# Optimization experiments

Hardware: AMD Instinct MI355X
Metric: run time of the kernel (lower is better)

The kernel has to match this reference:

```python
import jax, jax.numpy as jnp
import numpy as np

B, D = 8192, 1024          # batch, input dim
UNITS = [1024, 512]        # expert MLP hidden sizes
T, E_T, E_S = 2, 2, 4      # num_tasks, experts per task, shared experts
E = T * E_T + E_S          # total experts = 8


def setup_inputs() -> dict:
    key = jax.random.key(0)
    k = jax.random.split(key, 6)
    H, O = UNITS
    x = jax.random.normal(k[0], (B, D), dtype=jnp.float32)
    # glorot-normal-ish scaling for expert weights
    W1 = jax.random.normal(k[1], (E, D, H), dtype=jnp.float32) * np.sqrt(2.0 / (D + H))
    b1 = jnp.zeros((E, H), dtype=jnp.float32)
    W2 = jax.random.normal(k[2], (E, H, O), dtype=jnp.float32) * np.sqrt(2.0 / (H + O))
    b2 = jnp.zeros((E, O), dtype=jnp.float32)
    # per-task gate over (E_T + E_S) experts, no bias (use_bias=False in Dense)
    Wg = jax.random.normal(k[3], (T, D, E_T + E_S), dtype=jnp.float32) * np.sqrt(2.0 / (D + E_T + E_S))
    # shared gate over all E experts
    Wgs = jax.random.normal(k[4], (D, E), dtype=jnp.float32) * np.sqrt(2.0 / (D + E))
    return {"x": x, "W1": W1, "b1": b1, "W2": W2, "b2": b2, "Wg": Wg, "Wgs": Wgs}


def reference(x, W1, b1, W2, b2, Wg, Wgs):
    # All experts see the same input (2D-input path of CGC3: tf.tile over experts).
    # Batched grouped GEMM over the expert axis instead of a Python loop.
    h = jax.nn.relu(jnp.einsum('bd,edh->ebh', x, W1) + b1[:, None, :])   # [E,B,H]
    eo = jax.nn.relu(jnp.einsum('ebh,eho->ebo', h, W2) + b2[:, None, :]) # [E,B,O]

    outs = []
    for i in range(T):
        # experts for task i = its own E_T experts + the last E_S shared experts
        idx = jnp.array(list(range(i * E_T, (i + 1) * E_T)) + list(range(E - E_S, E)))
        g = jax.nn.softmax(x @ Wg[i], axis=-1)            # [B, E_T+E_S]
        sel = eo[idx]                                     # [E_T+E_S, B, O]
        outs.append(jnp.einsum('be,ebo->bo', g, sel))     # [B, O]
    # output_share=True: share tower gated over all experts
    gs = jax.nn.softmax(x @ Wgs, axis=-1)                 # [B, E]
    outs.append(jnp.einsum('be,ebo->bo', gs, eo))         # [B, O]
    return jnp.stack(outs, axis=1)                        # [B, T+1, O]
```

## Files before the change

### kernel.cpp

```cpp
#include <hip/hip_runtime.h>
#include <hip/hip_bf16.h>
#include <stdint.h>

#define B_SZ 8192
#define D_SZ 1024
#define H_SZ 1024
#define O_SZ 512
#define E_SZ 8

typedef float f32x4 __attribute__((ext_vector_type(4)));
typedef __bf16 bf16x8 __attribute__((ext_vector_type(8)));

typedef __attribute__((address_space(1))) uint32_t gu32;
typedef __attribute__((address_space(3))) uint32_t lu32;

__device__ __forceinline__ unsigned short f2bf(float f) {
    union { __hip_bfloat16 h; unsigned short u; } c;
    c.h = __float2bfloat16(f);
    return c.u;
}
__device__ __forceinline__ float bf2f(unsigned short u) {
    union { float f; uint32_t u; } c;
    c.u = ((uint32_t)u) << 16;
    return c.f;
}

__global__ __launch_bounds__(256) void k_convert_gates(const float* __restrict__ x,
                                                       const float* __restrict__ Wg,
                                                       const float* __restrict__ Wgs,
                                                       unsigned short* __restrict__ x_bf,
                                                       float* __restrict__ g_all) {
    const int wv = threadIdx.x >> 6;
    const int lane = threadIdx.x & 63;
    const int b = blockIdx.x * 4 + wv;
    const float* xr = x + (size_t)b * D_SZ;
    unsigned short* xo = x_bf + (size_t)b * D_SZ;
    float acc[20];
#pragma unroll
    for (int j = 0; j < 20; ++j) acc[j] = 0.f;
#pragma unroll 4
    for (int it = 0; it < 16; ++it) {
        const int d = it * 64 + lane;
        const float xv = xr[d];
        xo[d] = f2bf(xv);
        const float* w0 = Wg + (size_t)d * 6;
        const float* w1 = Wg + (size_t)D_SZ * 6 + (size_t)d * 6;
        const float* ws = Wgs + (size_t)d * 8;
#pragma unroll
        for (int j = 0; j < 6; ++j) acc[j] += xv * w0[j];
#pragma unroll
        for (int j = 0; j < 6; ++j) acc[6 + j] += xv * w1[j];
#pragma unroll
        for (int j = 0; j < 8; ++j) acc[12 + j] += xv * ws[j];
    }
#pragma unroll
    for (int j = 0; j < 20; ++j) {
        float v = acc[j];
#pragma unroll
        for (int s = 32; s > 0; s >>= 1) v += __shfl_down(v, s, 64);
        acc[j] = v;
    }
    if (lane == 0) {
        float* g = g_all + (size_t)b * 20;
#pragma unroll
        for (int t = 0; t < 3; ++t) {
            int base = (t == 0) ? 0 : (t == 1 ? 6 : 12);
            int cnt  = (t == 2) ? 8 : 6;
            float m = -1e30f;
            for (int j = 0; j < cnt; ++j) m = fmaxf(m, acc[base + j]);
            float ex[8]; float sum = 0.f;
            for (int j = 0; j < cnt; ++j) { ex[j] = __expf(acc[base + j] - m); sum += ex[j]; }
            float inv = 1.f / sum;
            for (int j = 0; j < cnt; ++j) g[base + j] = ex[j] * inv;
        }
    }
}

__global__ __launch_bounds__(512) void k_transpose_convert(const float* __restrict__ in,
                                                           unsigned short* __restrict__ out,
                                                           int R, int C) {
    __shared__ float tile[64][65];
    const float* src = in + (size_t)blockIdx.z * R * C;
    unsigned short* dst = out + (size_t)blockIdx.z * R * C;
    int c0 = blockIdx.x * 64, r0 = blockIdx.y * 64;
    int tx = threadIdx.x, ty = threadIdx.y;
#pragma unroll
    for (int rr = ty; rr < 64; rr += 8)
        tile[rr][tx] = src[(size_t)(r0 + rr) * C + c0 + tx];
    __syncthreads();
#pragma unroll
    for (int rr = ty; rr < 64; rr += 8)
        dst[(size_t)(c0 + rr) * R + r0 + tx] = f2bf(tile[tx][rr]);
}

__global__ __launch_bounds__(512, 2) void k_gemm_pipe(
    const unsigned short* __restrict__ A,
    const unsigned short* __restrict__ Bt,
    const float* __restrict__ bias,
    unsigned short* __restrict__ C,
    int M, int N, int K,
    long long sA, long long sB, long long sBias, long long sC, int e_base) {

    const int tid = threadIdx.x;
    const int lane = tid & 63, wid = tid >> 6;
    const int wr = wid >> 2, wc = wid & 3;
    const int lr = lane & 15, lg = lane >> 4;

    const int nwg = gridDim.x;
    const int wg = blockIdx.x;
    const int swz = (wg & 7) * (nwg >> 3) + (wg >> 3);
    const int nx = N >> 8;
    const int my = M >> 8;
    const int bx = swz % nx;
    const int t1 = swz / nx;
    const int by = t1 % my;
    const int e  = t1 / my + e_base;

    A    += (size_t)((long long)e * sA);
    Bt   += (size_t)((long long)e * sB);
    bias += (size_t)((long long)e * sBias);
    C    += (size_t)((long long)e * sC);

    const int m0 = by * 256, n0 = bx * 256;

    __shared__ __align__(16) unsigned short lds[65536];
    char* ldsb = (char*)lds;

    const int srow = tid >> 2;
    const int scol = (((tid & 3) ^ ((tid >> 3) & 3)) * 8);
    const int sdst = tid * 16;

    auto stageA2 = [&](int t) {
        const int bb = (t & 3) * 32768;
        const unsigned short* s0 = A + (size_t)(m0 + srow) * K + (t << 5) + scol;
        __builtin_amdgcn_global_load_lds((gu32*)s0, (lu32*)(ldsb + bb + sdst), 16, 0, 0);
        __builtin_amdgcn_global_load_lds((gu32*)(s0 + (size_t)128 * K),
                                         (lu32*)(ldsb + bb + 8192 + sdst), 16, 0, 0);
    };
    auto stageB2 = [&](int t) {
        const int bb = (t & 3) * 32768 + 16384;
        const unsigned short* s0 = Bt + (size_t)(n0 + srow) * K + (t << 5) + scol;
        __builtin_amdgcn_global_load_lds((gu32*)s0, (lu32*)(ldsb + bb + sdst), 16, 0, 0);
        __builtin_amdgcn_global_load_lds((gu32*)(s0 + (size_t)128 * K),
                                         (lu32*)(ldsb + bb + 8192 + sdst), 16, 0, 0);
    };

    const int cblk = (lg ^ ((lr >> 1) & 3)) * 16;
    const int aoff = wr * 8192 + lr * 64 + cblk;
    const int boff = 16384 + (wc >> 1) * 8192 + (wc & 1) * 4096 + lr * 64 + cblk;

    f32x4 acc[8][4];
#pragma unroll
    for (int i = 0; i < 8; ++i)
#pragma unroll
        for (int j = 0; j < 4; ++j)
            acc[i][j] = f32x4{0.f, 0.f, 0.f, 0.f};

    auto mfma16 = [&](const bf16x8 (&fa)[4], const bf16x8 (&fb)[4], int rbase) {
        __builtin_amdgcn_s_setprio(1);
#pragma unroll
        for (int i = 0; i < 4; ++i)
#pragma unroll
            for (int j = 0; j < 4; ++j)
                acc[rbase + i][j] = __builtin_amdgcn_mfma_f32_16x16x32_bf16(
                    fa[i], fb[j], acc[rbase + i][j], 0, 0, 0);
        __builtin_amdgcn_s_setprio(0);
    };

    const int NT = K >> 5;

    stageA2(0); stageB2(0); stageA2(1); stageB2(1); stageA2(2); stageB2(2);
    asm volatile("s_waitcnt vmcnt(8)" ::: "memory");
    asm volatile("s_barrier" ::: "memory");

    bf16x8 aU0[4], aL0[4], b0[4], aU1[4], aL1[4], b1v[4];
#pragma unroll
    for (int i = 0; i < 4; ++i) aU0[i] = *(const bf16x8*)(ldsb + aoff + i * 1024);
#pragma unroll
    for (int j = 0; j < 4; ++j) b0[j]  = *(const bf16x8*)(ldsb + boff + j * 1024);

    for (int t = 0; t < NT; t += 2) {
        const int bb0 = (t & 3) * 32768;
        const int bb1 = ((t + 1) & 3) * 32768;
        const int bb2 = ((t + 2) & 3) * 32768;

#pragma unroll
        for (int i = 0; i < 4; ++i) aL0[i] = *(const bf16x8*)(ldsb + bb0 + aoff + (4 + i) * 1024);
        if (t + 2 < NT) { asm volatile("s_waitcnt vmcnt(4)" ::: "memory"); }
        else            { asm volatile("s_waitcnt vmcnt(0)" ::: "memory"); }
        asm volatile("s_barrier" ::: "memory");
        if (t + 3 < NT) stageA2(t + 3);
        mfma16(aU0, b0, 0);

#pragma unroll
        for (int i = 0; i < 4; ++i) aU1[i] = *(const bf16x8*)(ldsb + bb1 + aoff + i * 1024);
#pragma unroll
        for (int j = 0; j < 4; ++j) b1v[j] = *(const bf16x8*)(ldsb + bb1 + boff + j * 1024);
        asm volatile("s_barrier" ::: "memory");
        if (t + 3 < NT) stageB2(t + 3);
        mfma16(aL0, b0, 4);

#pragma unroll
        for (int i = 0; i < 4; ++i) aL1[i] = *(const bf16x8*)(ldsb + bb1 + aoff + (4 + i) * 1024);
        if (t + 3 < NT) { asm volatile("s_waitcnt vmcnt(4)" ::: "memory"); }
        else            { asm volatile("s_waitcnt vmcnt(0)" ::: "memory"); }
        asm volatile("s_barrier" ::: "memory");
        if (t + 4 < NT) stageA2(t + 4);
        mfma16(aU1, b1v, 0);

        if (t + 2 < NT) {
#pragma unroll
            for (int i = 0; i < 4; ++i) aU0[i] = *(const bf16x8*)(ldsb + bb2 + aoff + i * 1024);
#pragma unroll
            for (int j = 0; j < 4; ++j) b0[j]  = *(const bf16x8*)(ldsb + bb2 + boff + j * 1024);
        }
        asm volatile("s_barrier" ::: "memory");
        if (t + 4 < NT) stageB2(t + 4);
        mfma16(aL1, b1v, 4);
    }

    __syncthreads();
    unsigned short* ct = (unsigned short*)ldsb;
#pragma unroll
    for (int j = 0; j < 4; ++j) {
        const int nn = wc * 64 + j * 16 + lr;
        const float bv = bias[n0 + nn];
#pragma unroll
        for (int i = 0; i < 8; ++i) {
            const int mb = wr * 128 + i * 16 + lg * 4;
#pragma unroll
            for (int r = 0; r < 4; ++r) {
                float v = fmaxf(acc[i][j][r] + bv, 0.f);
                ct[(size_t)(mb + r) * 256 + nn] = f2bf(v);
            }
        }
    }
    __syncthreads();
#pragma unroll
    for (int it = 0; it < 16; ++it) {
        const int row = it * 16 + (tid >> 5);
        const int colE = (tid & 31) * 8;
        *(int4*)(&C[(size_t)(m0 + row) * N + n0 + colE]) =
            *(const int4*)(ldsb + it * 8192 + (size_t)tid * 16);
    }
}

__global__ __launch_bounds__(256) void k_combine(const unsigned short* __restrict__ eo,
                                                 const float* __restrict__ g_all,
                                                 float* __restrict__ out) {
    int idx4 = blockIdx.x * 256 + threadIdx.x;
    int b = idx4 >> 7;
    int o4 = (idx4 & 127) * 4;
    const float* g = g_all + (size_t)b * 20;
    float v[E_SZ][4];
#pragma unroll
    for (int e = 0; e < E_SZ; ++e) {
        ushort4 u = *(const ushort4*)(eo + (size_t)e * B_SZ * O_SZ + (size_t)b * O_SZ + o4);
        v[e][0] = bf2f(u.x); v[e][1] = bf2f(u.y); v[e][2] = bf2f(u.z); v[e][3] = bf2f(u.w);
    }
    float4 r0, r1, r2;
    float* p0 = (float*)&r0; float* p1 = (float*)&r1; float* p2 = (float*)&r2;
#pragma unroll
    for (int c = 0; c < 4; ++c) {
        p0[c] = g[0] * v[0][c] + g[1] * v[1][c] + g[2] * v[4][c] + g[3] * v[5][c]
              + g[4] * v[6][c] + g[5] * v[7][c];
        p1[c] = g[6] * v[2][c] + g[7] * v[3][c] + g[8] * v[4][c] + g[9] * v[5][c]
              + g[10] * v[6][c] + g[11] * v[7][c];
        float s = 0.f;
#pragma unroll
        for (int e = 0; e < E_SZ; ++e) s += g[12 + e] * v[e][c];
        p2[c] = s;
    }
    size_t ob = (size_t)b * (3 * O_SZ) + o4;
    *(float4*)(out + ob) = r0;
    *(float4*)(out + ob + O_SZ) = r1;
    *(float4*)(out + ob + 2 * O_SZ) = r2;
}

extern "C" void kernel_launch(void* const* d_in, const int* in_sizes, int n_in,
                              void* d_out, int out_size, void* d_ws, size_t ws_size,
                              hipStream_t stream) {
    const float* x   = (const float*)d_in[0];
    const float* W1  = (const float*)d_in[1];
    const float* b1  = (const float*)d_in[2];
    const float* W2  = (const float*)d_in[3];
    const float* b2  = (const float*)d_in[4];
    const float* Wg  = (const float*)d_in[5];
    const float* Wgs = (const float*)d_in[6];
    float* out = (float*)d_out;

    char* ws = (char*)d_ws;
    const size_t SZ_XBF  = (size_t)B_SZ * D_SZ * 2;
    const size_t SZ_W1T  = (size_t)E_SZ * H_SZ * D_SZ * 2;
    const size_t SZ_W2T  = (size_t)E_SZ * O_SZ * H_SZ * 2;
    const size_t SZ_EO   = (size_t)E_SZ * B_SZ * O_SZ * 2;
    const size_t SZ_G    = (size_t)B_SZ * 20 * 4;
    const size_t SZ_HBIG = (size_t)E_SZ * B_SZ * H_SZ * 2;

    unsigned short* x_bf = (unsigned short*)ws;              ws += SZ_XBF;
    unsigned short* W1T  = (unsigned short*)ws;              ws += SZ_W1T;
    unsigned short* W2T  = (unsigned short*)ws;              ws += SZ_W2T;
    unsigned short* eo   = (unsigned short*)ws;              ws += SZ_EO;
    float* g_all         = (float*)ws;                       ws += SZ_G;
    unsigned short* h_buf = (unsigned short*)ws;

    const size_t fixed = SZ_XBF + SZ_W1T + SZ_W2T + SZ_EO + SZ_G;
    const bool big = ws_size >= fixed + SZ_HBIG;

    k_convert_gates<<<B_SZ / 4, 256, 0, stream>>>(x, Wg, Wgs, x_bf, g_all);
    dim3 tb(64, 8);
    k_transpose_convert<<<dim3(H_SZ / 64, D_SZ / 64, E_SZ), tb, 0, stream>>>(W1, W1T, D_SZ, H_SZ);
    k_transpose_convert<<<dim3(O_SZ / 64, H_SZ / 64, E_SZ), tb, 0, stream>>>(W2, W2T, H_SZ, O_SZ);

    if (big) {
        k_gemm_pipe<<<(H_SZ / 256) * (B_SZ / 256) * E_SZ, 512, 0, stream>>>(
            x_bf, W1T, b1, h_buf, B_SZ, H_SZ, D_SZ,
            0LL, (long long)H_SZ * D_SZ, (long long)H_SZ, (long long)B_SZ * H_SZ, 0);
        k_gemm_pipe<<<(O_SZ / 256) * (B_SZ / 256) * E_SZ, 512, 0, stream>>>(
            h_buf, W2T, b2, eo, B_SZ, O_SZ, H_SZ,
            (long long)B_SZ * H_SZ, (long long)O_SZ * H_SZ, (long long)O_SZ, (long long)B_SZ * O_SZ, 0);
    } else {
        for (int e = 0; e < E_SZ; ++e) {
            k_gemm_pipe<<<(H_SZ / 256) * (B_SZ / 256), 512, 0, stream>>>(
                x_bf, W1T, b1, h_buf, B_SZ, H_SZ, D_SZ,
                0LL, (long long)H_SZ * D_SZ, (long long)H_SZ, 0LL, e);
            k_gemm_pipe<<<(O_SZ / 256) * (B_SZ / 256), 512, 0, stream>>>(
                h_buf, W2T, b2, eo, B_SZ, O_SZ, H_SZ,
                0LL, (long long)O_SZ * H_SZ, (long long)O_SZ, (long long)B_SZ * O_SZ, e);
        }
    }

    k_combine<<<(B_SZ * O_SZ / 4) / 256, 256, 0, stream>>>(eo, g_all, out);
}
```

Baseline: 307.0 us.

## Use k-blocked panel layouts for GEMM operands and switch to 32x32x16 MFMA

Stores x, the transposed weights and the hidden activations in a panel layout (256-row panels of 8-element k-blocks), so each GEMM tile stage is one contiguous load into LDS. It also replaces the 16x16x32 MFMA tiles with 32x32x16 ones, using fewer, larger accumulators. The first GEMM now writes its output in panel layout through a swizzled LDS staging area so the second GEMM can read it the same way. The aim is cheaper global-to-LDS traffic and fewer LDS fragment reads per MFMA. The LDS read patterns change and may bring bank conflicts, and the layouts of all producers and consumers must agree exactly.

```diff
diff --git a/kernel.cpp b/kernel.cpp
--- a/kernel.cpp
+++ b/kernel.cpp
@@ -8,7 +8,7 @@
 #define O_SZ 512
 #define E_SZ 8
 
-typedef float f32x4 __attribute__((ext_vector_type(4)));
+typedef float f32x16 __attribute__((ext_vector_type(16)));
 typedef __bf16 bf16x8 __attribute__((ext_vector_type(8)));
 
 typedef __attribute__((address_space(1))) uint32_t gu32;
@@ -25,16 +25,18 @@
     return c.f;
 }
 
-__global__ __launch_bounds__(256) void k_convert_gates(const float* __restrict__ x,
-                                                       const float* __restrict__ Wg,
-                                                       const float* __restrict__ Wgs,
-                                                       unsigned short* __restrict__ x_bf,
-                                                       float* __restrict__ g_all) {
+
+__global__ __launch_bounds__(1024) void k_convert_gates(const float* __restrict__ x,
+                                                        const float* __restrict__ Wg,
+                                                        const float* __restrict__ Wgs,
+                                                        unsigned short* __restrict__ x_kb,
+                                                        float* __restrict__ g_all) {
+    __shared__ unsigned short xs[16][D_SZ];
     const int wv = threadIdx.x >> 6;
     const int lane = threadIdx.x & 63;
-    const int b = blockIdx.x * 4 + wv;
+    const int b0 = blockIdx.x * 16;
+    const int b = b0 + wv;
     const float* xr = x + (size_t)b * D_SZ;
-    unsigned short* xo = x_bf + (size_t)b * D_SZ;
     float acc[20];
 #pragma unroll
     for (int j = 0; j < 20; ++j) acc[j] = 0.f;
@@ -42,7 +44,7 @@
     for (int it = 0; it < 16; ++it) {
         const int d = it * 64 + lane;
         const float xv = xr[d];
-        xo[d] = f2bf(xv);
+        xs[wv][d] = f2bf(xv);
         const float* w0 = Wg + (size_t)d * 6;
         const float* w1 = Wg + (size_t)D_SZ * 6 + (size_t)d * 6;
         const float* ws = Wgs + (size_t)d * 8;
@@ -74,11 +76,21 @@
             for (int j = 0; j < cnt; ++j) g[base + j] = ex[j] * inv;
         }
     }
-}
-
-__global__ __launch_bounds__(512) void k_transpose_convert(const float* __restrict__ in,
-                                                           unsigned short* __restrict__ out,
-                                                           int R, int C) {
+    __syncthreads();
+    const char* lb = (const char*)&xs[0][0];
+#pragma unroll
+    for (int p = 0; p < 2; ++p) {
+        const int u = p * 1024 + threadIdx.x;
+        const int kblk = u >> 4, r16 = u & 15;
+        int4 v = *(const int4*)(lb + r16 * 2048 + kblk * 16);
+        *(int4*)(x_kb + (size_t)(b0 >> 8) * (D_SZ * 256) + (size_t)kblk * 2048
+                 + ((b0 & 255) + r16) * 8) = v;
+    }
+}
+
+__global__ __launch_bounds__(512) void k_transpose_panel(const float* __restrict__ in,
+                                                         unsigned short* __restrict__ out,
+                                                         int R, int C) {
     __shared__ float tile[64][65];
     const float* src = in + (size_t)blockIdx.z * R * C;
     unsigned short* dst = out + (size_t)blockIdx.z * R * C;
@@ -88,12 +100,17 @@
     for (int rr = ty; rr < 64; rr += 8)
         tile[rr][tx] = src[(size_t)(r0 + rr) * C + c0 + tx];
     __syncthreads();
-#pragma unroll
-    for (int rr = ty; rr < 64; rr += 8)
-        dst[(size_t)(c0 + rr) * R + r0 + tx] = f2bf(tile[tx][rr]);
-}
-
-__global__ __launch_bounds__(512, 2) void k_gemm_pipe(
+    union { ushort4 h[2]; int4 q; } u;
+#pragma unroll
+    for (int s = 0; s < 8; ++s)
+        ((unsigned short*)&u)[s] = f2bf(tile[ty * 8 + s][tx]);
+    const int c = c0 + tx;
+    *(int4*)(dst + (size_t)(c >> 8) * (R * 256) + (size_t)((r0 >> 3) + ty) * 2048
+             + (c & 255) * 8) = u.q;
+}
+
+template <bool PANEL_OUT>
+__global__ __launch_bounds__(512, 2) void k_gemm_p(
     const unsigned short* __restrict__ A,
     const unsigned short* __restrict__ Bt,
     const float* __restrict__ bias,
@@ -104,7 +121,7 @@
     const int tid = threadIdx.x;
     const int lane = tid & 63, wid = tid >> 6;
     const int wr = wid >> 2, wc = wid & 3;
-    const int lr = lane & 15, lg = lane >> 4;
+    const int lr32 = lane & 31, hi = lane >> 5;
 
     const int nwg = gridDim.x;
     const int wg = blockIdx.x;
@@ -126,122 +143,142 @@
     __shared__ __align__(16) unsigned short lds[65536];
     char* ldsb = (char*)lds;
 
-    const int srow = tid >> 2;
-    const int scol = (((tid & 3) ^ ((tid >> 3) & 3)) * 8);
-    const int sdst = tid * 16;
-
-    auto stageA2 = [&](int t) {
-        const int bb = (t & 3) * 32768;
-        const unsigned short* s0 = A + (size_t)(m0 + srow) * K + (t << 5) + scol;
-        __builtin_amdgcn_global_load_lds((gu32*)s0, (lu32*)(ldsb + bb + sdst), 16, 0, 0);
-        __builtin_amdgcn_global_load_lds((gu32*)(s0 + (size_t)128 * K),
-                                         (lu32*)(ldsb + bb + 8192 + sdst), 16, 0, 0);
-    };
-    auto stageB2 = [&](int t) {
-        const int bb = (t & 3) * 32768 + 16384;
-        const unsigned short* s0 = Bt + (size_t)(n0 + srow) * K + (t << 5) + scol;
-        __builtin_amdgcn_global_load_lds((gu32*)s0, (lu32*)(ldsb + bb + sdst), 16, 0, 0);
-        __builtin_amdgcn_global_load_lds((gu32*)(s0 + (size_t)128 * K),
-                                         (lu32*)(ldsb + bb + 8192 + sdst), 16, 0, 0);
-    };
-
-    const int cblk = (lg ^ ((lr >> 1) & 3)) * 16;
-    const int aoff = wr * 8192 + lr * 64 + cblk;
-    const int boff = 16384 + (wc >> 1) * 8192 + (wc & 1) * 4096 + lr * 64 + cblk;
-
-    f32x4 acc[8][4];
-#pragma unroll
-    for (int i = 0; i < 8; ++i)
-#pragma unroll
-        for (int j = 0; j < 4; ++j)
-            acc[i][j] = f32x4{0.f, 0.f, 0.f, 0.f};
-
-    auto mfma16 = [&](const bf16x8 (&fa)[4], const bf16x8 (&fb)[4], int rbase) {
+    const int skb = tid >> 8;
+    const int srw = tid & 255;
+
+    auto stageA = [&](int tt) {
+        const int bb = (tt & 3) * 32768;
+        const unsigned short* s0 = A + (size_t)(m0 >> 8) * K * 256
+                                     + (size_t)(tt * 4 + skb) * 2048 + srw * 8;
+        __builtin_amdgcn_global_load_lds((gu32*)s0, (lu32*)(ldsb + bb + tid * 16), 16, 0, 0);
+        __builtin_amdgcn_global_load_lds((gu32*)(s0 + 4096),
+                                         (lu32*)(ldsb + bb + 8192 + tid * 16), 16, 0, 0);
+    };
+    auto stageB = [&](int tt) {
+        const int bb = (tt & 3) * 32768 + 16384;
+        const unsigned short* s0 = Bt + (size_t)(n0 >> 8) * K * 256
+                                      + (size_t)(tt * 4 + skb) * 2048 + srw * 8;
+        __builtin_amdgcn_global_load_lds((gu32*)s0, (lu32*)(ldsb + bb + tid * 16), 16, 0, 0);
+        __builtin_amdgcn_global_load_lds((gu32*)(s0 + 4096),
+                                         (lu32*)(ldsb + bb + 8192 + tid * 16), 16, 0, 0);
+    };
+
+    const int abase = (wr * 128 + lr32) * 16 + hi * 4096;
+    const int bbase = 16384 + (wc * 64 + lr32) * 16 + hi * 4096;
+
+    auto readA = [&](bf16x8* d, int bb, int mb) {
+#pragma unroll
+        for (int q = 0; q < 4; ++q) {
+            const int mi = mb + (q >> 1), s = q & 1;
+            d[q] = *(const bf16x8*)(ldsb + bb + abase + mi * 512 + s * 8192);
+        }
+    };
+    auto readB = [&](bf16x8* d, int bb) {
+#pragma unroll
+        for (int q = 0; q < 4; ++q) {
+            const int nj = q >> 1, s = q & 1;
+            d[q] = *(const bf16x8*)(ldsb + bb + bbase + nj * 512 + s * 8192);
+        }
+    };
+
+    f32x16 acc[4][2];
+#pragma unroll
+    for (int i = 0; i < 4; ++i)
+#pragma unroll
+        for (int j = 0; j < 2; ++j)
+            acc[i][j] = (f32x16)(0.f);
+
+    auto mfma8 = [&](const bf16x8* fa, const bf16x8* fb, int rb) {
         __builtin_amdgcn_s_setprio(1);
 #pragma unroll
-        for (int i = 0; i < 4; ++i)
-#pragma unroll
-            for (int j = 0; j < 4; ++j)
-                acc[rbase + i][j] = __builtin_amdgcn_mfma_f32_16x16x32_bf16(
-                    fa[i], fb[j], acc[rbase + i][j], 0, 0, 0);
+        for (int i = 0; i < 2; ++i)
+#pragma unroll
+            for (int j = 0; j < 2; ++j)
+#pragma unroll
+                for (int s = 0; s < 2; ++s)
+                    acc[rb + i][j] = __builtin_amdgcn_mfma_f32_32x32x16_bf16(
+                        fa[i * 2 + s], fb[j * 2 + s], acc[rb + i][j], 0, 0, 0);
         __builtin_amdgcn_s_setprio(0);
     };
 
     const int NT = K >> 5;
 
-    stageA2(0); stageB2(0); stageA2(1); stageB2(1); stageA2(2); stageB2(2);
+    stageA(0); stageB(0); stageA(1); stageB(1); stageA(2); stageB(2);
     asm volatile("s_waitcnt vmcnt(8)" ::: "memory");
     asm volatile("s_barrier" ::: "memory");
 
     bf16x8 aU0[4], aL0[4], b0[4], aU1[4], aL1[4], b1v[4];
-#pragma unroll
-    for (int i = 0; i < 4; ++i) aU0[i] = *(const bf16x8*)(ldsb + aoff + i * 1024);
-#pragma unroll
-    for (int j = 0; j < 4; ++j) b0[j]  = *(const bf16x8*)(ldsb + boff + j * 1024);
+    readA(aU0, 0, 0); readB(b0, 0);
 
     for (int t = 0; t < NT; t += 2) {
         const int bb0 = (t & 3) * 32768;
         const int bb1 = ((t + 1) & 3) * 32768;
         const int bb2 = ((t + 2) & 3) * 32768;
 
-#pragma unroll
-        for (int i = 0; i < 4; ++i) aL0[i] = *(const bf16x8*)(ldsb + bb0 + aoff + (4 + i) * 1024);
+        readA(aL0, bb0, 2);
         if (t + 2 < NT) { asm volatile("s_waitcnt vmcnt(4)" ::: "memory"); }
         else            { asm volatile("s_waitcnt vmcnt(0)" ::: "memory"); }
         asm volatile("s_barrier" ::: "memory");
-        if (t + 3 < NT) stageA2(t + 3);
-        mfma16(aU0, b0, 0);
-
-#pragma unroll
-        for (int i = 0; i < 4; ++i) aU1[i] = *(const bf16x8*)(ldsb + bb1 + aoff + i * 1024);
-#pragma unroll
-        for (int j = 0; j < 4; ++j) b1v[j] = *(const bf16x8*)(ldsb + bb1 + boff + j * 1024);
+        if (t + 3 < NT) stageA(t + 3);
+        mfma8(aU0, b0, 0);
+
+        readA(aU1, bb1, 0); readB(b1v, bb1);
         asm volatile("s_barrier" ::: "memory");
-        if (t + 3 < NT) stageB2(t + 3);
-        mfma16(aL0, b0, 4);
-
-#pragma unroll
-        for (int i = 0; i < 4; ++i) aL1[i] = *(const bf16x8*)(ldsb + bb1 + aoff + (4 + i) * 1024);
+        if (t + 3 < NT) stageB(t + 3);
+        mfma8(aL0, b0, 2);
+
+        readA(aL1, bb1, 2);
         if (t + 3 < NT) { asm volatile("s_waitcnt vmcnt(4)" ::: "memory"); }
         else            { asm volatile("s_waitcnt vmcnt(0)" ::: "memory"); }
         asm volatile("s_barrier" ::: "memory");
-        if (t + 4 < NT) stageA2(t + 4);
-        mfma16(aU1, b1v, 0);
-
-        if (t + 2 < NT) {
-#pragma unroll
-            for (int i = 0; i < 4; ++i) aU0[i] = *(const bf16x8*)(ldsb + bb2 + aoff + i * 1024);
-#pragma unroll
-            for (int j = 0; j < 4; ++j) b0[j]  = *(const bf16x8*)(ldsb + bb2 + boff + j * 1024);
-        }
+        if (t + 4 < NT) stageA(t + 4);
+        mfma8(aU1, b1v, 0);
+
+        if (t + 2 < NT) { readA(aU0, bb2, 0); readB(b0, bb2); }
         asm volatile("s_barrier" ::: "memory");
-        if (t + 4 < NT) stageB2(t + 4);
-        mfma16(aL1, b1v, 4);
+        if (t + 4 < NT) stageB(t + 4);
+        mfma8(aL1, b1v, 4 - 2);
     }
 
     __syncthreads();
     unsigned short* ct = (unsigned short*)ldsb;
 #pragma unroll
-    for (int j = 0; j < 4; ++j) {
-        const int nn = wc * 64 + j * 16 + lr;
+    for (int nj = 0; nj < 2; ++nj) {
+        const int nn = wc * 64 + nj * 32 + lr32;
         const float bv = bias[n0 + nn];
 #pragma unroll
-        for (int i = 0; i < 8; ++i) {
-            const int mb = wr * 128 + i * 16 + lg * 4;
-#pragma unroll
-            for (int r = 0; r < 4; ++r) {
-                float v = fmaxf(acc[i][j][r] + bv, 0.f);
-                ct[(size_t)(mb + r) * 256 + nn] = f2bf(v);
+        for (int mi = 0; mi < 4; ++mi) {
+#pragma unroll
+            for (int r = 0; r < 16; ++r) {
+                const int mloc = wr * 128 + mi * 32 + (r & 3) + 8 * (r >> 2) + 4 * hi;
+                float v = fmaxf(acc[mi][nj][r] + bv, 0.f);
+                if (PANEL_OUT) {
+                    const int pu = (nn >> 3) ^ (mloc & 7);
+                    *(unsigned short*)(ldsb + mloc * 512 + pu * 16 + (nn & 7) * 2) = f2bf(v);
+                } else {
+                    ct[(size_t)mloc * 256 + nn] = f2bf(v);
+                }
             }
         }
     }
     __syncthreads();
-#pragma unroll
-    for (int it = 0; it < 16; ++it) {
-        const int row = it * 16 + (tid >> 5);
-        const int colE = (tid & 31) * 8;
-        *(int4*)(&C[(size_t)(m0 + row) * N + n0 + colE]) =
-            *(const int4*)(ldsb + it * 8192 + (size_t)tid * 16);
+    if (PANEL_OUT) {
+#pragma unroll
+        for (int it = 0; it < 16; ++it) {
+            const int u = it * 512 + tid;
+            const int blk = u >> 8, row = u & 255;
+            int4 v = *(const int4*)(ldsb + row * 512 + ((blk ^ (row & 7)) * 16));
+            *(int4*)(C + (size_t)(m0 >> 8) * N * 256 + (size_t)((n0 >> 3) + blk) * 2048
+                     + row * 8) = v;
+        }
+    } else {
+#pragma unroll
+        for (int it = 0; it < 16; ++it) {
+            const int row = it * 16 + (tid >> 5);
+            const int colE = (tid & 31) * 8;
+            *(int4*)(&C[(size_t)(m0 + row) * N + n0 + colE]) =
+                *(const int4*)(ldsb + it * 8192 + (size_t)tid * 16);
+        }
     }
 }
 
@@ -297,7 +334,7 @@
     const size_t SZ_G    = (size_t)B_SZ * 20 * 4;
     const size_t SZ_HBIG = (size_t)E_SZ * B_SZ * H_SZ * 2;
 
-    unsigned short* x_bf = (unsigned short*)ws;              ws += SZ_XBF;
+    unsigned short* x_kb = (unsigned short*)ws;              ws += SZ_XBF;
     unsigned short* W1T  = (unsigned short*)ws;              ws += SZ_W1T;
     unsigned short* W2T  = (unsigned short*)ws;              ws += SZ_W2T;
     unsigned short* eo   = (unsigned short*)ws;              ws += SZ_EO;
@@ -307,24 +344,24 @@
     const size_t fixed = SZ_XBF + SZ_W1T + SZ_W2T + SZ_EO + SZ_G;
     const bool big = ws_size >= fixed + SZ_HBIG;
 
-    k_convert_gates<<<B_SZ / 4, 256, 0, stream>>>(x, Wg, Wgs, x_bf, g_all);
+    k_convert_gates<<<B_SZ / 16, 1024, 0, stream>>>(x, Wg, Wgs, x_kb, g_all);
     dim3 tb(64, 8);
-    k_transpose_convert<<<dim3(H_SZ / 64, D_SZ / 64, E_SZ), tb, 0, stream>>>(W1, W1T, D_SZ, H_SZ);
-    k_transpose_convert<<<dim3(O_SZ / 64, H_SZ / 64, E_SZ), tb, 0, stream>>>(W2, W2T, H_SZ, O_SZ);
+    k_transpose_panel<<<dim3(H_SZ / 64, D_SZ / 64, E_SZ), tb, 0, stream>>>(W1, W1T, D_SZ, H_SZ);
+    k_transpose_panel<<<dim3(O_SZ / 64, H_SZ / 64, E_SZ), tb, 0, stream>>>(W2, W2T, H_SZ, O_SZ);
 
     if (big) {
-        k_gemm_pipe<<<(H_SZ / 256) * (B_SZ / 256) * E_SZ, 512, 0, stream>>>(
-            x_bf, W1T, b1, h_buf, B_SZ, H_SZ, D_SZ,
+        k_gemm_p<true><<<(H_SZ / 256) * (B_SZ / 256) * E_SZ, 512, 0, stream>>>(
+            x_kb, W1T, b1, h_buf, B_SZ, H_SZ, D_SZ,
             0LL, (long long)H_SZ * D_SZ, (long long)H_SZ, (long long)B_SZ * H_SZ, 0);
-        k_gemm_pipe<<<(O_SZ / 256) * (B_SZ / 256) * E_SZ, 512, 0, stream>>>(
+        k_gemm_p<false><<<(O_SZ / 256) * (B_SZ / 256) * E_SZ, 512, 0, stream>>>(
             h_buf, W2T, b2, eo, B_SZ, O_SZ, H_SZ,
             (long long)B_SZ * H_SZ, (long long)O_SZ * H_SZ, (long long)O_SZ, (long long)B_SZ * O_SZ, 0);
     } else {
         for (int e = 0; e < E_SZ; ++e) {
-            k_gemm_pipe<<<(H_SZ / 256) * (B_SZ / 256), 512, 0, stream>>>(
-                x_bf, W1T, b1, h_buf, B_SZ, H_SZ, D_SZ,
+            k_gemm_p<true><<<(H_SZ / 256) * (B_SZ / 256), 512, 0, stream>>>(
+                x_kb, W1T, b1, h_buf, B_SZ, H_SZ, D_SZ,
                 0LL, (long long)H_SZ * D_SZ, (long long)H_SZ, 0LL, e);
-            k_gemm_pipe<<<(O_SZ / 256) * (B_SZ / 256), 512, 0, stream>>>(
+            k_gemm_p<false><<<(O_SZ / 256) * (B_SZ / 256), 512, 0, stream>>>(
                 h_buf, W2T, b2, eo, B_SZ, O_SZ, H_SZ,
                 0LL, (long long)O_SZ * H_SZ, (long long)O_SZ, (long long)B_SZ * O_SZ, e);
         }
```

Result: slower. 315.6 us (+2.8%).

## Compute gate logits with MFMA, merge weight transposes, widen combine vectors

Applied to the files above, without the earlier changes.

Splits the old fused convert+gates kernel into a plain vectorized x-to-bf16 conversion and a separate gate kernel. The gate kernel stages the gate weights as bf16 in LDS and computes the logits with 16x16x32 bf16 MFMA instead of per-lane scalar FMAs with strided global loads. The two weight transpose launches become one launch, and the combine kernel now processes 8 outputs per thread with 16-byte loads. The gate logits now use bf16 inputs and weights instead of fp32, which lowers softmax precision. Each gate block also reloads the full gate weight matrix from global memory.

```diff
diff --git a/kernel.cpp b/kernel.cpp
--- a/kernel.cpp
+++ b/kernel.cpp
@@ -25,63 +25,31 @@
     return c.f;
 }
 
-__global__ __launch_bounds__(256) void k_convert_gates(const float* __restrict__ x,
-                                                       const float* __restrict__ Wg,
-                                                       const float* __restrict__ Wgs,
-                                                       unsigned short* __restrict__ x_bf,
-                                                       float* __restrict__ g_all) {
-    const int wv = threadIdx.x >> 6;
-    const int lane = threadIdx.x & 63;
-    const int b = blockIdx.x * 4 + wv;
-    const float* xr = x + (size_t)b * D_SZ;
-    unsigned short* xo = x_bf + (size_t)b * D_SZ;
-    float acc[20];
-#pragma unroll
-    for (int j = 0; j < 20; ++j) acc[j] = 0.f;
-#pragma unroll 4
-    for (int it = 0; it < 16; ++it) {
-        const int d = it * 64 + lane;
-        const float xv = xr[d];
-        xo[d] = f2bf(xv);
-        const float* w0 = Wg + (size_t)d * 6;
-        const float* w1 = Wg + (size_t)D_SZ * 6 + (size_t)d * 6;
-        const float* ws = Wgs + (size_t)d * 8;
-#pragma unroll
-        for (int j = 0; j < 6; ++j) acc[j] += xv * w0[j];
-#pragma unroll
-        for (int j = 0; j < 6; ++j) acc[6 + j] += xv * w1[j];
-#pragma unroll
-        for (int j = 0; j < 8; ++j) acc[12 + j] += xv * ws[j];
-    }
-#pragma unroll
-    for (int j = 0; j < 20; ++j) {
-        float v = acc[j];
-#pragma unroll
-        for (int s = 32; s > 0; s >>= 1) v += __shfl_down(v, s, 64);
-        acc[j] = v;
-    }
-    if (lane == 0) {
-        float* g = g_all + (size_t)b * 20;
-#pragma unroll
-        for (int t = 0; t < 3; ++t) {
-            int base = (t == 0) ? 0 : (t == 1 ? 6 : 12);
-            int cnt  = (t == 2) ? 8 : 6;
-            float m = -1e30f;
-            for (int j = 0; j < cnt; ++j) m = fmaxf(m, acc[base + j]);
-            float ex[8]; float sum = 0.f;
-            for (int j = 0; j < cnt; ++j) { ex[j] = __expf(acc[base + j] - m); sum += ex[j]; }
-            float inv = 1.f / sum;
-            for (int j = 0; j < cnt; ++j) g[base + j] = ex[j] * inv;
-        }
-    }
-}
-
-__global__ __launch_bounds__(512) void k_transpose_convert(const float* __restrict__ in,
-                                                           unsigned short* __restrict__ out,
-                                                           int R, int C) {
+__global__ __launch_bounds__(256) void k_convert(const float* __restrict__ in,
+                                                 unsigned short* __restrict__ out, int n8) {
+    int i = blockIdx.x * 256 + threadIdx.x;
+    if (i >= n8) return;
+    const float4* p = (const float4*)in + (size_t)i * 2;
+    float4 a = p[0], b = p[1];
+    ushort4 lo, hi;
+    lo.x = f2bf(a.x); lo.y = f2bf(a.y); lo.z = f2bf(a.z); lo.w = f2bf(a.w);
+    hi.x = f2bf(b.x); hi.y = f2bf(b.y); hi.z = f2bf(b.z); hi.w = f2bf(b.w);
+    ushort4* q = (ushort4*)out + (size_t)i * 2;
+    q[0] = lo; q[1] = hi;
+}
+
+__global__ __launch_bounds__(512) void k_transpose_both(const float* __restrict__ W1,
+                                                        unsigned short* __restrict__ W1T,
+                                                        const float* __restrict__ W2,
+                                                        unsigned short* __restrict__ W2T) {
+    const int z = blockIdx.z;
+    const float* in; unsigned short* out; int R, C, e;
+    if (z < 8) { in = W1; out = W1T; R = D_SZ; C = H_SZ; e = z; }
+    else       { in = W2; out = W2T; R = H_SZ; C = O_SZ; e = z - 8;
+                 if ((int)blockIdx.x >= C / 64) return; }
     __shared__ float tile[64][65];
-    const float* src = in + (size_t)blockIdx.z * R * C;
-    unsigned short* dst = out + (size_t)blockIdx.z * R * C;
+    const float* src = in + (size_t)e * R * C;
+    unsigned short* dst = out + (size_t)e * R * C;
     int c0 = blockIdx.x * 64, r0 = blockIdx.y * 64;
     int tx = threadIdx.x, ty = threadIdx.y;
 #pragma unroll
@@ -91,6 +59,64 @@
 #pragma unroll
     for (int rr = ty; rr < 64; rr += 8)
         dst[(size_t)(c0 + rr) * R + r0 + tx] = f2bf(tile[tx][rr]);
+}
+
+__global__ __launch_bounds__(256) void k_gates_mfma(const unsigned short* __restrict__ x_bf,
+                                                    const float* __restrict__ Wg,
+                                                    const float* __restrict__ Wgs,
+                                                    float* __restrict__ g_all) {
+    __shared__ unsigned short wlds[32 * 1032];
+    __shared__ float logits[32][24];
+    const int tid = threadIdx.x;
+
+    for (int idx = tid; idx < 32 * 1024; idx += 256) {
+        const int j = idx >> 10, k = idx & 1023;
+        float v = 0.f;
+        if (j < 6)       v = Wg[(size_t)k * 6 + j];
+        else if (j < 12) v = Wg[(size_t)D_SZ * 6 + (size_t)k * 6 + (j - 6)];
+        else if (j < 20) v = Wgs[(size_t)k * 8 + (j - 12)];
+        wlds[j * 1032 + k] = f2bf(v);
+    }
+    __syncthreads();
+
+    const int lane = tid & 63, w = tid >> 6;
+    const int rt = w >> 1, jt = w & 1;
+    const int lr = lane & 15, lg = lane >> 4;
+    const int row0 = blockIdx.x * 32 + rt * 16;
+
+    const unsigned short* xr = x_bf + (size_t)(row0 + lr) * D_SZ;
+    const unsigned short* wrow = &wlds[(jt * 16 + lr) * 1032];
+
+    f32x4 acc = f32x4{0.f, 0.f, 0.f, 0.f};
+#pragma unroll 4
+    for (int kt = 0; kt < 32; ++kt) {
+        bf16x8 a = *(const bf16x8*)(xr + kt * 32 + lg * 8);
+        bf16x8 b = *(const bf16x8*)(wrow + kt * 32 + lg * 8);
+        acc = __builtin_amdgcn_mfma_f32_16x16x32_bf16(a, b, acc, 0, 0, 0);
+    }
+    const int j = jt * 16 + lr;
+    if (j < 24) {
+#pragma unroll
+        for (int r = 0; r < 4; ++r)
+            logits[rt * 16 + lg * 4 + r][j] = acc[r];
+    }
+    __syncthreads();
+
+    if (tid < 32) {
+        const int row = tid;
+        float* g = g_all + (size_t)(blockIdx.x * 32 + row) * 20;
+#pragma unroll
+        for (int t = 0; t < 3; ++t) {
+            const int base = (t == 0) ? 0 : (t == 1 ? 6 : 12);
+            const int cnt  = (t == 2) ? 8 : 6;
+            float m = -1e30f;
+            for (int q = 0; q < cnt; ++q) m = fmaxf(m, logits[row][base + q]);
+            float ex[8]; float sum = 0.f;
+            for (int q = 0; q < cnt; ++q) { ex[q] = __expf(logits[row][base + q] - m); sum += ex[q]; }
+            float inv = 1.f / sum;
+            for (int q = 0; q < cnt; ++q) g[base + q] = ex[q] * inv;
+        }
+    }
 }
 
 __global__ __launch_bounds__(512, 2) void k_gemm_pipe(
@@ -248,33 +274,38 @@
 __global__ __launch_bounds__(256) void k_combine(const unsigned short* __restrict__ eo,
                                                  const float* __restrict__ g_all,
                                                  float* __restrict__ out) {
-    int idx4 = blockIdx.x * 256 + threadIdx.x;
-    int b = idx4 >> 7;
-    int o4 = (idx4 & 127) * 4;
+    int idx8 = blockIdx.x * 256 + threadIdx.x;
+    int b = idx8 >> 6;
+    int o8 = (idx8 & 63) * 8;
     const float* g = g_all + (size_t)b * 20;
-    float v[E_SZ][4];
+    float v[E_SZ][8];
 #pragma unroll
     for (int e = 0; e < E_SZ; ++e) {
-        ushort4 u = *(const ushort4*)(eo + (size_t)e * B_SZ * O_SZ + (size_t)b * O_SZ + o4);
-        v[e][0] = bf2f(u.x); v[e][1] = bf2f(u.y); v[e][2] = bf2f(u.z); v[e][3] = bf2f(u.w);
-    }
-    float4 r0, r1, r2;
-    float* p0 = (float*)&r0; float* p1 = (float*)&r1; float* p2 = (float*)&r2;
-#pragma unroll
-    for (int c = 0; c < 4; ++c) {
-        p0[c] = g[0] * v[0][c] + g[1] * v[1][c] + g[2] * v[4][c] + g[3] * v[5][c]
+        const unsigned short* p = eo + (size_t)e * B_SZ * O_SZ + (size_t)b * O_SZ + o8;
+        int4 u = *(const int4*)p;
+        const unsigned short* us = (const unsigned short*)&u;
+#pragma unroll
+        for (int c = 0; c < 8; ++c) v[e][c] = bf2f(us[c]);
+    }
+    float r0[8], r1[8], r2[8];
+#pragma unroll
+    for (int c = 0; c < 8; ++c) {
+        r0[c] = g[0] * v[0][c] + g[1] * v[1][c] + g[2] * v[4][c] + g[3] * v[5][c]
               + g[4] * v[6][c] + g[5] * v[7][c];
-        p1[c] = g[6] * v[2][c] + g[7] * v[3][c] + g[8] * v[4][c] + g[9] * v[5][c]
+        r1[c] = g[6] * v[2][c] + g[7] * v[3][c] + g[8] * v[4][c] + g[9] * v[5][c]
               + g[10] * v[6][c] + g[11] * v[7][c];
         float s = 0.f;
 #pragma unroll
         for (int e = 0; e < E_SZ; ++e) s += g[12 + e] * v[e][c];
-        p2[c] = s;
-    }
-    size_t ob = (size_t)b * (3 * O_SZ) + o4;
-    *(float4*)(out + ob) = r0;
-    *(float4*)(out + ob + O_SZ) = r1;
-    *(float4*)(out + ob + 2 * O_SZ) = r2;
+        r2[c] = s;
+    }
+    size_t ob = (size_t)b * (3 * O_SZ) + o8;
+    *(float4*)(out + ob)             = *(float4*)&r0[0];
+    *(float4*)(out + ob + 4)         = *(float4*)&r0[4];
+    *(float4*)(out + ob + O_SZ)      = *(float4*)&r1[0];
+    *(float4*)(out + ob + O_SZ + 4)  = *(float4*)&r1[4];
+    *(float4*)(out + ob + 2 * O_SZ)  = *(float4*)&r2[0];
+    *(float4*)(out + ob + 2 * O_SZ + 4) = *(float4*)&r2[4];
 }
 
 extern "C" void kernel_launch(void* const* d_in, const int* in_sizes, int n_in,
@@ -307,10 +338,9 @@
     const size_t fixed = SZ_XBF + SZ_W1T + SZ_W2T + SZ_EO + SZ_G;
     const bool big = ws_size >= fixed + SZ_HBIG;
 
-    k_convert_gates<<<B_SZ / 4, 256, 0, stream>>>(x, Wg, Wgs, x_bf, g_all);
-    dim3 tb(64, 8);
-    k_transpose_convert<<<dim3(H_SZ / 64, D_SZ / 64, E_SZ), tb, 0, stream>>>(W1, W1T, D_SZ, H_SZ);
-    k_transpose_convert<<<dim3(O_SZ / 64, H_SZ / 64, E_SZ), tb, 0, stream>>>(W2, W2T, H_SZ, O_SZ);
+    k_convert<<<(B_SZ * D_SZ / 8 + 255) / 256, 256, 0, stream>>>(x, x_bf, B_SZ * D_SZ / 8);
+    k_transpose_both<<<dim3(16, 16, 16), dim3(64, 8), 0, stream>>>(W1, W1T, W2, W2T);
+    k_gates_mfma<<<B_SZ / 32, 256, 0, stream>>>(x_bf, Wg, Wgs, g_all);
 
     if (big) {
         k_gemm_pipe<<<(H_SZ / 256) * (B_SZ / 256) * E_SZ, 512, 0, stream>>>(
@@ -330,5 +360,5 @@
         }
     }
 
-    k_combine<<<(B_SZ * O_SZ / 4) / 256, 256, 0, stream>>>(eo, g_all, out);
-}
+    k_combine<<<(B_SZ * O_SZ / 8) / 256, 256, 0, stream>>>(eo, g_all, out);
+}
```

After: 303.2 us. No clear change (-1.3%).
